# Kernel tuning notes

Hardware: AMD Instinct MI355X
Metric: run time of the kernel (lower is better)

## Reference

```python
import jax, jax.numpy as jnp
import numpy as np

B, N, D, H = 4, 2048, 256, 8
DK = D // H
SCALE = np.sqrt(DK).astype(np.float32)


def setup_inputs() -> dict:
    key = jax.random.key(0)
    ks = jax.random.split(key, 8)
    s = 1.0 / np.sqrt(D)
    return {
        "x": jax.random.normal(ks[0], (B, N, D), jnp.float32),
        "edge_weights": jax.random.normal(ks[1], (B, N, N), jnp.float32),
        "mask": jax.random.randint(ks[2], (B, N, N), 0, 2, jnp.int32),
        "w_q": jax.random.normal(ks[3], (D, D), jnp.float32) * s,
        "w_k": jax.random.normal(ks[4], (D, D), jnp.float32) * s,
        "w_v": jax.random.normal(ks[5], (D, D), jnp.float32) * s,
        "w_o": jax.random.normal(ks[6], (D, D), jnp.float32) * s,
        "b_o": jax.random.normal(ks[7], (D,), jnp.float32) * s,
    }


def reference(x, edge_weights, mask, w_q, w_k, w_v, w_o, b_o):
    # torch Linear: y = x @ W.T ; split into heads -> [B, H, N, DK]
    def split_heads(t):
        return t.reshape(B, N, H, DK).transpose(0, 2, 1, 3)

    Q = split_heads(x @ w_q.T)
    K = split_heads(x @ w_k.T)
    V = split_heads(x @ w_v.T)

    scores = jnp.einsum("bhnd,bhmd->bhnm", Q, K) / SCALE
    scores = scores + edge_weights[:, None, :, :]
    scores = jnp.where(mask[:, None, :, :] == 0, jnp.float32(-1e9), scores)
    attn = jax.nn.softmax(scores, axis=-1)  # dropout is identity in eval
    out = jnp.einsum("bhnm,bhmd->bhnd", attn, V)
    out = out.transpose(0, 2, 1, 3).reshape(B, N, D)
    return out @ w_o.T + b_o
```

## Files before the change

### kernel.cpp

```cpp
#include <hip/hip_runtime.h>

#define LOG2E 1.4426950408889634f
#define NEGBIG -3.0e38f

typedef float  f32x4  __attribute__((ext_vector_type(4)));
typedef float  f32x16 __attribute__((ext_vector_type(16)));
typedef short  bf16x8 __attribute__((ext_vector_type(8)));
typedef unsigned short u16x4 __attribute__((ext_vector_type(4)));
typedef int    i32x4  __attribute__((ext_vector_type(4)));
typedef unsigned int u32x2 __attribute__((ext_vector_type(2)));

__device__ __forceinline__ unsigned short f2bf(float f) {
  union { float f; unsigned u; } v; v.f = f;
  unsigned r = v.u + 0x7FFFu + ((v.u >> 16) & 1u);
  return (unsigned short)(r >> 16);
}

__device__ __forceinline__ unsigned cvtpk(float a, float b) {
  unsigned r;
  asm("v_cvt_pk_bf16_f32 %0, %1, %2" : "=v"(r) : "v"(a), "v"(b));
  return r;
}

__device__ __forceinline__ bf16x8 load_cvt8(const float* p) {
  f32x4 a = *(const f32x4*)p;
  f32x4 b = *(const f32x4*)(p + 4);
  bf16x8 r;
  r[0]=(short)f2bf(a[0]); r[1]=(short)f2bf(a[1]); r[2]=(short)f2bf(a[2]); r[3]=(short)f2bf(a[3]);
  r[4]=(short)f2bf(b[0]); r[5]=(short)f2bf(b[1]); r[6]=(short)f2bf(b[2]); r[7]=(short)f2bf(b[3]);
  return r;
}

__global__ __launch_bounds__(256) void qkv_kernel(
    const float* __restrict__ x,
    const float* __restrict__ wq, const float* __restrict__ wk, const float* __restrict__ wv,
    unsigned short* __restrict__ Qo, unsigned short* __restrict__ Ko,
    unsigned short* __restrict__ Vto)
{
  const int mode = blockIdx.y;
  const int n0   = blockIdx.x * 64;
  const int b    = n0 >> 11;
  const int nl0  = n0 & 2047;
  const int wave = threadIdx.x >> 6;
  const int lane = threadIdx.x & 63;
  const int li = lane & 15, qt = lane >> 4;

  f32x4 acc[4][4];
#pragma unroll
  for (int i = 0; i < 4; i++)
#pragma unroll
    for (int j = 0; j < 4; j++) acc[i][j] = (f32x4)0.0f;

  if (mode < 2) {
    const float* w = mode ? wk : wq;
    const float osc = mode ? 1.0f : (1.4426950408889634f / 5.656854249492381f);
#pragma unroll
    for (int ks = 0; ks < 8; ks++) {
      bf16x8 af[4], bfr[4];
#pragma unroll
      for (int dm = 0; dm < 4; dm++)
        af[dm] = load_cvt8(w + (size_t)(wave*64 + dm*16 + li)*256 + ks*32 + qt*8);
#pragma unroll
      for (int nf = 0; nf < 4; nf++)
        bfr[nf] = load_cvt8(x + (size_t)(n0 + nf*16 + li)*256 + ks*32 + qt*8);
#pragma unroll
      for (int dm = 0; dm < 4; dm++)
#pragma unroll
        for (int nf = 0; nf < 4; nf++)
          acc[dm][nf] = __builtin_amdgcn_mfma_f32_16x16x32_bf16(af[dm], bfr[nf], acc[dm][nf], 0, 0, 0);
    }
#pragma unroll
    for (int dm = 0; dm < 4; dm++) {
      const int dbase = wave*64 + dm*16 + qt*4;
      const int h = dbase >> 5, dk = dbase & 31;
#pragma unroll
      for (int nf = 0; nf < 4; nf++) {
        const int nl = nl0 + nf*16 + li;
        u16x4 o;
#pragma unroll
        for (int r = 0; r < 4; r++) o[r] = f2bf(acc[dm][nf][r] * osc);
        if (mode == 0) {
          *(u16x4*)(Qo + ((size_t)(b*8 + h)*2048 + nl)*32 + dk) = o;
        } else {
          const size_t addr = (size_t)(b*8 + h)*65536
              + (size_t)(nl >> 5)*1024 + (size_t)((dk >> 4) & 1)*512
              + (size_t)((nl & 31) + 32*((dk >> 3) & 1))*8 + (dk & 7);
          *(u16x4*)(Ko + addr) = o;
        }
      }
    }
  } else {
#pragma unroll
    for (int ks = 0; ks < 8; ks++) {
      bf16x8 af[4], bfr[4];
#pragma unroll
      for (int nm = 0; nm < 4; nm++)
        af[nm] = load_cvt8(x + (size_t)(n0 + nm*16 + li)*256 + ks*32 + qt*8);
#pragma unroll
      for (int df = 0; df < 4; df++)
        bfr[df] = load_cvt8(wv + (size_t)(wave*64 + df*16 + li)*256 + ks*32 + qt*8);
#pragma unroll
      for (int nm = 0; nm < 4; nm++)
#pragma unroll
        for (int df = 0; df < 4; df++)
          acc[nm][df] = __builtin_amdgcn_mfma_f32_16x16x32_bf16(af[nm], bfr[df], acc[nm][df], 0, 0, 0);
    }
#pragma unroll
    for (int nm = 0; nm < 4; nm++) {
      const int nl = nl0 + nm*16 + qt*4;
#pragma unroll
      for (int df = 0; df < 4; df++) {
        const int d = wave*64 + df*16 + li;
        const int h = d >> 5, dv = d & 31;
        u16x4 o;
#pragma unroll
        for (int r = 0; r < 4; r++) o[r] = f2bf(acc[nm][df][r]);
        const size_t addr = (size_t)(b*8 + h)*65536
            + (size_t)(nl >> 5)*1024 + (size_t)((nl >> 4) & 1)*512
            + (size_t)(((nl >> 3) & 1)*32 + dv)*8 + (nl & 7);
        *(u16x4*)(Vto + addr) = o;
      }
    }
  }
}

__global__ __launch_bounds__(512, 2) void attn_kernel(
    const unsigned short* __restrict__ Qg,
    const unsigned short* __restrict__ Kf,
    const unsigned short* __restrict__ Vf,
    const float* __restrict__ edge,
    const int*   __restrict__ mask,
    unsigned short* __restrict__ Og)
{
  __shared__ __attribute__((aligned(16))) float me_s[2][4096];

  const int bid = blockIdx.x;
  const int b  = (bid >> 1) & 3;
  const int qi = ((bid >> 3) << 1) | (bid & 1);
  const int q0 = qi * 32;
  const int tid  = threadIdx.x;
  const int wave = tid >> 6;
  const int lane = tid & 63;
  const int ql = lane & 31, hi = lane >> 5;
  const int h = wave;

  const unsigned short* qbase = Qg + ((size_t)(b*8 + h)*2048 + q0)*32;
  const unsigned short* kf = Kf + (size_t)(b*8 + h)*65536 + lane*8;
  const unsigned short* vf = Vf + (size_t)(b*8 + h)*65536 + lane*8;

  const int q_s = tid >> 4;
  const int k4  = (tid & 15) * 4;
  const float* eaddr = edge + ((size_t)b*2048 + q0 + q_s)*2048 + k4;
  const int*   maddr = mask + ((size_t)b*2048 + q0 + q_s)*2048 + k4;
  const int sC2  = (((k4 & 31) >> 3) * 2) + ((k4 >> 2) & 1);
  const int widx = (k4 >> 5)*1024 + (sC2*32 + (q_s ^ sC2))*4;
  int rix[4];
#pragma unroll
  for (int rg = 0; rg < 4; rg++) {
    const int C2 = rg*2 + hi;
    rix[rg] = (C2*32 + (ql ^ C2)) * 4;
  }

  const bf16x8 qf0 = *(const bf16x8*)(qbase + (size_t)ql*32 +  0 + hi*8);
  const bf16x8 qf1 = *(const bf16x8*)(qbase + (size_t)ql*32 + 16 + hi*8);

  {
    f32x4 e0 = *(const f32x4*)eaddr;
    i32x4 m0 = *(const i32x4*)maddr;
    f32x4 e1 = *(const f32x4*)(eaddr + 64);
    i32x4 m1 = *(const i32x4*)(maddr + 64);
    f32x4 v0, v1;
#pragma unroll
    for (int r = 0; r < 4; r++) v0[r] = m0[r] ? e0[r]*LOG2E : NEGBIG;
#pragma unroll
    for (int r = 0; r < 4; r++) v1[r] = m1[r] ? e1[r]*LOG2E : NEGBIG;
    *(f32x4*)&me_s[0][widx] = v0;
    *(f32x4*)&me_s[0][widx + 2048] = v1;
  }
  __syncthreads();

  f32x4 se0 = *(const f32x4*)(eaddr + 128);
  i32x4 sm0 = *(const i32x4*)(maddr + 128);
  f32x4 se1 = *(const f32x4*)(eaddr + 192);
  i32x4 sm1 = *(const i32x4*)(maddr + 192);

  bf16x8 kXa = *(const bf16x8*)(kf);
  bf16x8 kXb = *(const bf16x8*)(kf + 512);
  bf16x8 kYa, kYb;

  float lsum = 0.f;
  f32x16 oacc = (f32x16)0.0f;

  union CU { f32x16 v; f32x4 q[4]; };

#define PV_KS(SV, HALF, VA)                                                   \
  {                                                                           \
    unsigned a0 = cvtpk(SV[(HALF)*8+0], SV[(HALF)*8+1]);                      \
    unsigned a1 = cvtpk(SV[(HALF)*8+2], SV[(HALF)*8+3]);                      \
    unsigned b0 = cvtpk(SV[(HALF)*8+4], SV[(HALF)*8+5]);                      \
    unsigned b1 = cvtpk(SV[(HALF)*8+6], SV[(HALF)*8+7]);                      \
    u32x2 p0 = __builtin_amdgcn_permlane32_swap(a0, b0, false, false);        \
    u32x2 p1 = __builtin_amdgcn_permlane32_swap(a1, b1, false, false);        \
    i32x4 pw4;                                                                \
    pw4[0] = (int)p0[0]; pw4[1] = (int)p1[0];                                 \
    pw4[2] = (int)p0[1]; pw4[3] = (int)p1[1];                                 \
    const bf16x8 pf = __builtin_bit_cast(bf16x8, pw4);                        \
    oacc = __builtin_amdgcn_mfma_f32_32x32x16_bf16(VA, pf, oacc, 0, 0, 0);    \
  }

#define GROUP(KB, T, KCa, KCb, KNa, KNb)                                      \
  {                                                                           \
    const size_t nxt = (size_t)(((KB) + 1) & 63) * 1024;                      \
    KNa = *(const bf16x8*)(kf + nxt);                                         \
    KNb = *(const bf16x8*)(kf + nxt + 512);                                   \
    const bf16x8 vA0 = *(const bf16x8*)(vf + (size_t)(KB)*1024);              \
    const bf16x8 vA1 = *(const bf16x8*)(vf + (size_t)(KB)*1024 + 512);        \
    CU c;                                                                     \
    _Pragma("unroll")                                                         \
    for (int rg = 0; rg < 4; rg++)                                            \
      c.q[rg] = *(const f32x4*)(mb + (T)*1024 + rix[rg]);                     \
    f32x16 s = __builtin_amdgcn_mfma_f32_32x32x16_bf16(KCa, qf0, c.v, 0, 0, 0); \
    s = __builtin_amdgcn_mfma_f32_32x32x16_bf16(KCb, qf1, s, 0, 0, 0);        \
    _Pragma("unroll")                                                         \
    for (int i = 0; i < 16; i++) s[i] = __builtin_amdgcn_exp2f(s[i]);         \
    {                                                                         \
      float r0 = 0.f, r1 = 0.f, r2 = 0.f, r3 = 0.f;                           \
      _Pragma("unroll")                                                       \
      for (int i = 0; i < 4; i++) {                                           \
        r0 += s[4*i]; r1 += s[4*i+1]; r2 += s[4*i+2]; r3 += s[4*i+3];         \
      }                                                                       \
      lsum += (r0 + r1) + (r2 + r3);                                          \
    }                                                                         \
    PV_KS(s, 0, vA0)                                                          \
    PV_KS(s, 1, vA1)                                                          \
  }

  for (int p = 0; p < 16; ++p) {
    const float* mb = &me_s[p & 1][0];
    if (p < 15) {
      f32x4 v0, v1;
#pragma unroll
      for (int r = 0; r < 4; r++) v0[r] = sm0[r] ? se0[r]*LOG2E : NEGBIG;
#pragma unroll
      for (int r = 0; r < 4; r++) v1[r] = sm1[r] ? se1[r]*LOG2E : NEGBIG;
      *(f32x4*)&me_s[(p + 1) & 1][widx] = v0;
      *(f32x4*)&me_s[(p + 1) & 1][widx + 2048] = v1;
    }
    if (p < 14) {
      se0 = *(const f32x4*)(eaddr + (p + 2)*128);
      sm0 = *(const i32x4*)(maddr + (p + 2)*128);
      se1 = *(const f32x4*)(eaddr + (p + 2)*128 + 64);
      sm1 = *(const i32x4*)(maddr + (p + 2)*128 + 64);
    }
    const int g0 = p * 4;
    GROUP(g0,     0, kXa, kXb, kYa, kYb)
    GROUP(g0 + 1, 1, kYa, kYb, kXa, kXb)
    GROUP(g0 + 2, 2, kXa, kXb, kYa, kYb)
    GROUP(g0 + 3, 3, kYa, kYb, kXa, kXb)
    __syncthreads();
  }
#undef GROUP
#undef PV_KS

  const float ltot = lsum + __shfl_xor(lsum, 32);
  const float rl = 1.0f / ltot;
#pragma unroll
  for (int rg = 0; rg < 4; rg++) {
    u16x4 o;
#pragma unroll
    for (int r = 0; r < 4; r++) o[r] = f2bf(oacc[rg*4 + r] * rl);
    *(u16x4*)(Og + ((size_t)(b*2048 + q0 + ql))*256 + h*32 + rg*8 + hi*4) = o;
  }
}

__global__ __launch_bounds__(256) void proj_kernel(
    const unsigned short* __restrict__ O,
    const float* __restrict__ wo, const float* __restrict__ bo,
    float* __restrict__ Y)
{
  const int n0   = blockIdx.x * 64;
  const int wave = threadIdx.x >> 6;
  const int lane = threadIdx.x & 63;
  const int li = lane & 15, qt = lane >> 4;

  f32x4 acc[4][4];
#pragma unroll
  for (int i = 0; i < 4; i++)
#pragma unroll
    for (int j = 0; j < 4; j++) acc[i][j] = (f32x4)0.0f;

#pragma unroll
  for (int ks = 0; ks < 8; ks++) {
    bf16x8 af[4], bfr[4];
#pragma unroll
    for (int dm = 0; dm < 4; dm++)
      af[dm] = load_cvt8(wo + (size_t)(wave*64 + dm*16 + li)*256 + ks*32 + qt*8);
#pragma unroll
    for (int nf = 0; nf < 4; nf++)
      bfr[nf] = *(const bf16x8*)(O + (size_t)(n0 + nf*16 + li)*256 + ks*32 + qt*8);
#pragma unroll
    for (int dm = 0; dm < 4; dm++)
#pragma unroll
      for (int nf = 0; nf < 4; nf++)
        acc[dm][nf] = __builtin_amdgcn_mfma_f32_16x16x32_bf16(af[dm], bfr[nf], acc[dm][nf], 0, 0, 0);
  }

#pragma unroll
  for (int dm = 0; dm < 4; dm++) {
    const int d0 = wave*64 + dm*16 + qt*4;
    const f32x4 bo4 = *(const f32x4*)(bo + d0);
#pragma unroll
    for (int nf = 0; nf < 4; nf++) {
      const int n = n0 + nf*16 + li;
      f32x4 y = acc[dm][nf] + bo4;
      *(f32x4*)(Y + (size_t)n*256 + d0) = y;
    }
  }
}

extern "C" void kernel_launch(void* const* d_in, const int* in_sizes, int n_in,
                              void* d_out, int out_size, void* d_ws, size_t ws_size,
                              hipStream_t stream) {
  const float* x  = (const float*)d_in[0];
  const float* ew = (const float*)d_in[1];
  const int*   mk = (const int*)d_in[2];
  const float* wq = (const float*)d_in[3];
  const float* wk = (const float*)d_in[4];
  const float* wv = (const float*)d_in[5];
  const float* wo = (const float*)d_in[6];
  const float* bo = (const float*)d_in[7];
  float* y = (float*)d_out;

  unsigned short* Q  = (unsigned short*)d_ws;
  unsigned short* Kf = Q  + 2097152;
  unsigned short* Vf = Kf + 2097152;
  unsigned short* O  = Vf + 2097152;

  qkv_kernel<<<dim3(128, 3), 256, 0, stream>>>(x, wq, wk, wv, Q, Kf, Vf);
  attn_kernel<<<256, 512, 0, stream>>>(Q, Kf, Vf, ew, mk, O);
  proj_kernel<<<128, 256, 0, stream>>>(O, wo, bo, y);
}
```

Before: 94.97 us.

## Split attention block into two four-head halves with 256 threads each

The attention kernel now launches 512 blocks of 256 threads instead of 256 blocks of 512. Each block handles four heads for its 32-query tile, selected by the low block-id bit. Each thread stages twice as many edge/mask elements into shared memory so the 256 threads still fill the same tile. This gives finer-grained blocks and possibly better occupancy or scheduling. In exchange, every edge/mask tile is now read and converted by two blocks instead of one, doubling that global traffic and conversion work.

```diff
diff --git a/kernel.cpp b/kernel.cpp
--- a/kernel.cpp
+++ b/kernel.cpp
@@ -124,7 +124,7 @@
   }
 }
 
-__global__ __launch_bounds__(512, 2) void attn_kernel(
+__global__ __launch_bounds__(256, 2) void attn_kernel(
     const unsigned short* __restrict__ Qg,
     const unsigned short* __restrict__ Kf,
     const unsigned short* __restrict__ Vf,
@@ -136,13 +136,14 @@
 
   const int bid = blockIdx.x;
   const int b  = (bid >> 1) & 3;
-  const int qi = ((bid >> 3) << 1) | (bid & 1);
+  const int hg = bid & 1;
+  const int qi = bid >> 3;
   const int q0 = qi * 32;
   const int tid  = threadIdx.x;
   const int wave = tid >> 6;
   const int lane = tid & 63;
   const int ql = lane & 31, hi = lane >> 5;
-  const int h = wave;
+  const int h = hg*4 + wave;
 
   const unsigned short* qbase = Qg + ((size_t)(b*8 + h)*2048 + q0)*32;
   const unsigned short* kf = Kf + (size_t)(b*8 + h)*65536 + lane*8;
@@ -152,6 +153,8 @@
   const int k4  = (tid & 15) * 4;
   const float* eaddr = edge + ((size_t)b*2048 + q0 + q_s)*2048 + k4;
   const int*   maddr = mask + ((size_t)b*2048 + q0 + q_s)*2048 + k4;
+  const float* eaddr2 = eaddr + 16*2048;
+  const int*   maddr2 = maddr + 16*2048;
   const int sC2  = (((k4 & 31) >> 3) * 2) + ((k4 >> 2) & 1);
   const int widx = (k4 >> 5)*1024 + (sC2*32 + (q_s ^ sC2))*4;
   int rix[4];
@@ -164,25 +167,35 @@
   const bf16x8 qf0 = *(const bf16x8*)(qbase + (size_t)ql*32 +  0 + hi*8);
   const bf16x8 qf1 = *(const bf16x8*)(qbase + (size_t)ql*32 + 16 + hi*8);
 
+#define STAGE_CONV_WRITE(BUF, E00, M00, E10, M10, E01, M01, E11, M11)         \
+  {                                                                           \
+    f32x4 w00, w10, w01, w11;                                                 \
+    _Pragma("unroll")                                                         \
+    for (int r = 0; r < 4; r++) {                                             \
+      w00[r] = M00[r] ? E00[r]*LOG2E : NEGBIG;                                \
+      w10[r] = M10[r] ? E10[r]*LOG2E : NEGBIG;                                \
+      w01[r] = M01[r] ? E01[r]*LOG2E : NEGBIG;                                \
+      w11[r] = M11[r] ? E11[r]*LOG2E : NEGBIG;                                \
+    }                                                                         \
+    *(f32x4*)&me_s[BUF][widx]        = w00;                                   \
+    *(f32x4*)&me_s[BUF][widx + 64]   = w10;                                   \
+    *(f32x4*)&me_s[BUF][widx + 2048] = w01;                                   \
+    *(f32x4*)&me_s[BUF][widx + 2112] = w11;                                   \
+  }
+
   {
-    f32x4 e0 = *(const f32x4*)eaddr;
-    i32x4 m0 = *(const i32x4*)maddr;
-    f32x4 e1 = *(const f32x4*)(eaddr + 64);
-    i32x4 m1 = *(const i32x4*)(maddr + 64);
-    f32x4 v0, v1;
-#pragma unroll
-    for (int r = 0; r < 4; r++) v0[r] = m0[r] ? e0[r]*LOG2E : NEGBIG;
-#pragma unroll
-    for (int r = 0; r < 4; r++) v1[r] = m1[r] ? e1[r]*LOG2E : NEGBIG;
-    *(f32x4*)&me_s[0][widx] = v0;
-    *(f32x4*)&me_s[0][widx + 2048] = v1;
+    f32x4 e00 = *(const f32x4*)eaddr;        i32x4 m00 = *(const i32x4*)maddr;
+    f32x4 e10 = *(const f32x4*)eaddr2;       i32x4 m10 = *(const i32x4*)maddr2;
+    f32x4 e01 = *(const f32x4*)(eaddr + 64); i32x4 m01 = *(const i32x4*)(maddr + 64);
+    f32x4 e11 = *(const f32x4*)(eaddr2 + 64);i32x4 m11 = *(const i32x4*)(maddr2 + 64);
+    STAGE_CONV_WRITE(0, e00, m00, e10, m10, e01, m01, e11, m11)
   }
   __syncthreads();
 
-  f32x4 se0 = *(const f32x4*)(eaddr + 128);
-  i32x4 sm0 = *(const i32x4*)(maddr + 128);
-  f32x4 se1 = *(const f32x4*)(eaddr + 192);
-  i32x4 sm1 = *(const i32x4*)(maddr + 192);
+  f32x4 se00 = *(const f32x4*)(eaddr + 128);  i32x4 sm00 = *(const i32x4*)(maddr + 128);
+  f32x4 se10 = *(const f32x4*)(eaddr2 + 128); i32x4 sm10 = *(const i32x4*)(maddr2 + 128);
+  f32x4 se01 = *(const f32x4*)(eaddr + 192);  i32x4 sm01 = *(const i32x4*)(maddr + 192);
+  f32x4 se11 = *(const f32x4*)(eaddr2 + 192); i32x4 sm11 = *(const i32x4*)(maddr2 + 192);
 
   bf16x8 kXa = *(const bf16x8*)(kf);
   bf16x8 kXb = *(const bf16x8*)(kf + 512);
@@ -238,19 +251,14 @@
   for (int p = 0; p < 16; ++p) {
     const float* mb = &me_s[p & 1][0];
     if (p < 15) {
-      f32x4 v0, v1;
-#pragma unroll
-      for (int r = 0; r < 4; r++) v0[r] = sm0[r] ? se0[r]*LOG2E : NEGBIG;
-#pragma unroll
-      for (int r = 0; r < 4; r++) v1[r] = sm1[r] ? se1[r]*LOG2E : NEGBIG;
-      *(f32x4*)&me_s[(p + 1) & 1][widx] = v0;
-      *(f32x4*)&me_s[(p + 1) & 1][widx + 2048] = v1;
+      STAGE_CONV_WRITE((p + 1) & 1, se00, sm00, se10, sm10, se01, sm01, se11, sm11)
     }
     if (p < 14) {
-      se0 = *(const f32x4*)(eaddr + (p + 2)*128);
-      sm0 = *(const i32x4*)(maddr + (p + 2)*128);
-      se1 = *(const f32x4*)(eaddr + (p + 2)*128 + 64);
-      sm1 = *(const i32x4*)(maddr + (p + 2)*128 + 64);
+      const int ofs = (p + 2)*128;
+      se00 = *(const f32x4*)(eaddr + ofs);       sm00 = *(const i32x4*)(maddr + ofs);
+      se10 = *(const f32x4*)(eaddr2 + ofs);      sm10 = *(const i32x4*)(maddr2 + ofs);
+      se01 = *(const f32x4*)(eaddr + ofs + 64);  sm01 = *(const i32x4*)(maddr + ofs + 64);
+      se11 = *(const f32x4*)(eaddr2 + ofs + 64); sm11 = *(const i32x4*)(maddr2 + ofs + 64);
     }
     const int g0 = p * 4;
     GROUP(g0,     0, kXa, kXb, kYa, kYb)
@@ -261,6 +269,7 @@
   }
 #undef GROUP
 #undef PV_KS
+#undef STAGE_CONV_WRITE
 
   const float ltot = lsum + __shfl_xor(lsum, 32);
   const float rl = 1.0f / ltot;
@@ -337,6 +346,6 @@
   unsigned short* O  = Vf + 2097152;
 
   qkv_kernel<<<dim3(128, 3), 256, 0, stream>>>(x, wq, wk, wv, Q, Kf, Vf);
-  attn_kernel<<<256, 512, 0, stream>>>(Q, Kf, Vf, ew, mk, O);
+  attn_kernel<<<512, 256, 0, stream>>>(Q, Kf, Vf, ew, mk, O);
   proj_kernel<<<128, 256, 0, stream>>>(O, wo, bo, y);
 }
```

Result: slower. 103.8 us (+9.3%).

## Split attention key range across two wave groups per block and merge partials

Applied to the files above, without the earlier changes.

Doubles the attention block to 1024 threads: each head is served by two waves, each handling half of the key range, with separate staged edge/mask tiles in shared memory. At the end, the second-half waves write their partial output accumulators and row sums to LDS, and the first-half waves add them before normalising and storing. The aim is to halve the serial loop length per wave and raise latency hiding within a block. The cost is double the shared memory, one extra merge barrier, and launch bounds that allow only one block per CU, which may cap register use.

```diff
diff --git a/kernel.cpp b/kernel.cpp
--- a/kernel.cpp
+++ b/kernel.cpp
@@ -124,7 +124,7 @@
   }
 }
 
-__global__ __launch_bounds__(512, 2) void attn_kernel(
+__global__ __launch_bounds__(1024, 1) void attn_kernel(
     const unsigned short* __restrict__ Qg,
     const unsigned short* __restrict__ Kf,
     const unsigned short* __restrict__ Vf,
@@ -132,7 +132,7 @@
     const int*   __restrict__ mask,
     unsigned short* __restrict__ Og)
 {
-  __shared__ __attribute__((aligned(16))) float me_s[2][4096];
+  __shared__ __attribute__((aligned(16))) float me_s[2][2][4096];
 
   const int bid = blockIdx.x;
   const int b  = (bid >> 1) & 3;
@@ -142,16 +142,19 @@
   const int wave = tid >> 6;
   const int lane = tid & 63;
   const int ql = lane & 31, hi = lane >> 5;
-  const int h = wave;
+  const int h  = wave & 7;
+  const int kh = wave >> 3;
 
   const unsigned short* qbase = Qg + ((size_t)(b*8 + h)*2048 + q0)*32;
-  const unsigned short* kf = Kf + (size_t)(b*8 + h)*65536 + lane*8;
-  const unsigned short* vf = Vf + (size_t)(b*8 + h)*65536 + lane*8;
-
-  const int q_s = tid >> 4;
-  const int k4  = (tid & 15) * 4;
-  const float* eaddr = edge + ((size_t)b*2048 + q0 + q_s)*2048 + k4;
-  const int*   maddr = mask + ((size_t)b*2048 + q0 + q_s)*2048 + k4;
+  const unsigned short* kf = Kf + (size_t)(b*8 + h)*65536 + (size_t)kh*32768 + lane*8;
+  const unsigned short* vf = Vf + (size_t)(b*8 + h)*65536 + (size_t)kh*32768 + lane*8;
+
+  const int th  = tid >> 9;
+  const int t9  = tid & 511;
+  const int q_s = t9 >> 4;
+  const int k4  = (t9 & 15) * 4;
+  const float* eaddr = edge + ((size_t)b*2048 + q0 + q_s)*2048 + th*1024 + k4;
+  const int*   maddr = mask + ((size_t)b*2048 + q0 + q_s)*2048 + th*1024 + k4;
   const int sC2  = (((k4 & 31) >> 3) * 2) + ((k4 >> 2) & 1);
   const int widx = (k4 >> 5)*1024 + (sC2*32 + (q_s ^ sC2))*4;
   int rix[4];
@@ -174,8 +177,8 @@
     for (int r = 0; r < 4; r++) v0[r] = m0[r] ? e0[r]*LOG2E : NEGBIG;
 #pragma unroll
     for (int r = 0; r < 4; r++) v1[r] = m1[r] ? e1[r]*LOG2E : NEGBIG;
-    *(f32x4*)&me_s[0][widx] = v0;
-    *(f32x4*)&me_s[0][widx + 2048] = v1;
+    *(f32x4*)&me_s[0][th][widx] = v0;
+    *(f32x4*)&me_s[0][th][widx + 2048] = v1;
   }
   __syncthreads();
 
@@ -210,7 +213,7 @@
 
 #define GROUP(KB, T, KCa, KCb, KNa, KNb)                                      \
   {                                                                           \
-    const size_t nxt = (size_t)(((KB) + 1) & 63) * 1024;                      \
+    const size_t nxt = (size_t)(((KB) + 1) & 31) * 1024;                      \
     KNa = *(const bf16x8*)(kf + nxt);                                         \
     KNb = *(const bf16x8*)(kf + nxt + 512);                                   \
     const bf16x8 vA0 = *(const bf16x8*)(vf + (size_t)(KB)*1024);              \
@@ -235,22 +238,23 @@
     PV_KS(s, 1, vA1)                                                          \
   }
 
-  for (int p = 0; p < 16; ++p) {
-    const float* mb = &me_s[p & 1][0];
-    if (p < 15) {
+  for (int p = 0; p < 8; ++p) {
+    const float* mb = &me_s[p & 1][kh][0];
+    if (p < 7) {
       f32x4 v0, v1;
 #pragma unroll
       for (int r = 0; r < 4; r++) v0[r] = sm0[r] ? se0[r]*LOG2E : NEGBIG;
 #pragma unroll
       for (int r = 0; r < 4; r++) v1[r] = sm1[r] ? se1[r]*LOG2E : NEGBIG;
-      *(f32x4*)&me_s[(p + 1) & 1][widx] = v0;
-      *(f32x4*)&me_s[(p + 1) & 1][widx + 2048] = v1;
-    }
-    if (p < 14) {
-      se0 = *(const f32x4*)(eaddr + (p + 2)*128);
-      sm0 = *(const i32x4*)(maddr + (p + 2)*128);
-      se1 = *(const f32x4*)(eaddr + (p + 2)*128 + 64);
-      sm1 = *(const i32x4*)(maddr + (p + 2)*128 + 64);
+      *(f32x4*)&me_s[(p + 1) & 1][th][widx] = v0;
+      *(f32x4*)&me_s[(p + 1) & 1][th][widx + 2048] = v1;
+    }
+    if (p < 6) {
+      const int ofs = (p + 2)*128;
+      se0 = *(const f32x4*)(eaddr + ofs);
+      sm0 = *(const i32x4*)(maddr + ofs);
+      se1 = *(const f32x4*)(eaddr + ofs + 64);
+      sm1 = *(const i32x4*)(maddr + ofs + 64);
     }
     const int g0 = p * 4;
     GROUP(g0,     0, kXa, kXb, kYa, kYb)
@@ -262,14 +266,27 @@
 #undef GROUP
 #undef PV_KS
 
-  const float ltot = lsum + __shfl_xor(lsum, 32);
-  const float rl = 1.0f / ltot;
-#pragma unroll
-  for (int rg = 0; rg < 4; rg++) {
-    u16x4 o;
-#pragma unroll
-    for (int r = 0; r < 4; r++) o[r] = f2bf(oacc[rg*4 + r] * rl);
-    *(u16x4*)(Og + ((size_t)(b*2048 + q0 + ql))*256 + h*32 + rg*8 + hi*4) = o;
+  float* mrg = &me_s[0][0][0];
+  const int mbase = h*1088 + lane*17;
+  if (kh == 1) {
+#pragma unroll
+    for (int i = 0; i < 16; i++) mrg[mbase + i] = oacc[i];
+    mrg[mbase + 16] = lsum;
+  }
+  __syncthreads();
+  if (kh == 0) {
+#pragma unroll
+    for (int i = 0; i < 16; i++) oacc[i] += mrg[mbase + i];
+    lsum += mrg[mbase + 16];
+    const float ltot = lsum + __shfl_xor(lsum, 32);
+    const float rl = 1.0f / ltot;
+#pragma unroll
+    for (int rg = 0; rg < 4; rg++) {
+      u16x4 o;
+#pragma unroll
+      for (int r = 0; r < 4; r++) o[r] = f2bf(oacc[rg*4 + r] * rl);
+      *(u16x4*)(Og + ((size_t)(b*2048 + q0 + ql))*256 + h*32 + rg*8 + hi*4) = o;
+    }
   }
 }
 
@@ -337,6 +354,6 @@
   unsigned short* O  = Vf + 2097152;
 
   qkv_kernel<<<dim3(128, 3), 256, 0, stream>>>(x, wq, wk, wv, Q, Kf, Vf);
-  attn_kernel<<<256, 512, 0, stream>>>(Q, Kf, Vf, ew, mk, O);
+  attn_kernel<<<256, 1024, 0, stream>>>(Q, Kf, Vf, ew, mk, O);
   proj_kernel<<<128, 256, 0, stream>>>(O, wo, bo, y);
 }
```

Result: slower. 105.5 us (+11.1%).

## Fuse output projection into attention kernel epilogue via LDS-staged O tile

Applied to the files above, without the earlier changes.

Removes the separate proj_kernel launch and the global round-trip of the bf16 attention output. Each attention block writes its normalized 32x256 output tile to shared memory, synchronizes, and then its 8 waves compute a 32-column slice of the W_o projection plus bias directly to Y. This saves one kernel launch and the O write/read. In exchange, every block reloads and converts the fp32 W_o slice, and the extra LDS may reduce occupancy.

```diff
diff --git a/kernel.cpp b/kernel.cpp
--- a/kernel.cpp
+++ b/kernel.cpp
@@ -130,9 +130,12 @@
     const unsigned short* __restrict__ Vf,
     const float* __restrict__ edge,
     const int*   __restrict__ mask,
-    unsigned short* __restrict__ Og)
+    const float* __restrict__ wo,
+    const float* __restrict__ bo,
+    float* __restrict__ Y)
 {
   __shared__ __attribute__((aligned(16))) float me_s[2][4096];
+  __shared__ __attribute__((aligned(16))) unsigned short o_lds[32][264];
 
   const int bid = blockIdx.x;
   const int b  = (bid >> 1) & 3;
@@ -262,58 +265,51 @@
 #undef GROUP
 #undef PV_KS
 
-  const float ltot = lsum + __shfl_xor(lsum, 32);
-  const float rl = 1.0f / ltot;
-#pragma unroll
-  for (int rg = 0; rg < 4; rg++) {
-    u16x4 o;
-#pragma unroll
-    for (int r = 0; r < 4; r++) o[r] = f2bf(oacc[rg*4 + r] * rl);
-    *(u16x4*)(Og + ((size_t)(b*2048 + q0 + ql))*256 + h*32 + rg*8 + hi*4) = o;
-  }
-}
-
-__global__ __launch_bounds__(256) void proj_kernel(
-    const unsigned short* __restrict__ O,
-    const float* __restrict__ wo, const float* __restrict__ bo,
-    float* __restrict__ Y)
-{
-  const int n0   = blockIdx.x * 64;
-  const int wave = threadIdx.x >> 6;
-  const int lane = threadIdx.x & 63;
-  const int li = lane & 15, qt = lane >> 4;
-
-  f32x4 acc[4][4];
-#pragma unroll
-  for (int i = 0; i < 4; i++)
-#pragma unroll
-    for (int j = 0; j < 4; j++) acc[i][j] = (f32x4)0.0f;
-
-#pragma unroll
-  for (int ks = 0; ks < 8; ks++) {
-    bf16x8 af[4], bfr[4];
-#pragma unroll
-    for (int dm = 0; dm < 4; dm++)
-      af[dm] = load_cvt8(wo + (size_t)(wave*64 + dm*16 + li)*256 + ks*32 + qt*8);
-#pragma unroll
-    for (int nf = 0; nf < 4; nf++)
-      bfr[nf] = *(const bf16x8*)(O + (size_t)(n0 + nf*16 + li)*256 + ks*32 + qt*8);
-#pragma unroll
-    for (int dm = 0; dm < 4; dm++)
-#pragma unroll
-      for (int nf = 0; nf < 4; nf++)
-        acc[dm][nf] = __builtin_amdgcn_mfma_f32_16x16x32_bf16(af[dm], bfr[nf], acc[dm][nf], 0, 0, 0);
-  }
-
-#pragma unroll
-  for (int dm = 0; dm < 4; dm++) {
-    const int d0 = wave*64 + dm*16 + qt*4;
-    const f32x4 bo4 = *(const f32x4*)(bo + d0);
-#pragma unroll
-    for (int nf = 0; nf < 4; nf++) {
-      const int n = n0 + nf*16 + li;
-      f32x4 y = acc[dm][nf] + bo4;
-      *(f32x4*)(Y + (size_t)n*256 + d0) = y;
+  {
+    const float ltot = lsum + __shfl_xor(lsum, 32);
+    const float rl = 1.0f / ltot;
+#pragma unroll
+    for (int rg = 0; rg < 4; rg++) {
+      u16x4 o;
+#pragma unroll
+      for (int r = 0; r < 4; r++) o[r] = f2bf(oacc[rg*4 + r] * rl);
+      *(u16x4*)&o_lds[ql][h*32 + rg*8 + hi*4] = o;
+    }
+  }
+  __syncthreads();
+
+  {
+    const int li = lane & 15, qt = lane >> 4;
+    f32x4 acc2[2][2];
+#pragma unroll
+    for (int i = 0; i < 2; i++)
+#pragma unroll
+      for (int j = 0; j < 2; j++) acc2[i][j] = (f32x4)0.0f;
+#pragma unroll
+    for (int ks = 0; ks < 8; ks++) {
+      bf16x8 af[2], bfr[2];
+#pragma unroll
+      for (int df = 0; df < 2; df++)
+        af[df] = load_cvt8(wo + (size_t)(wave*32 + df*16 + li)*256 + ks*32 + qt*8);
+#pragma unroll
+      for (int nf = 0; nf < 2; nf++)
+        bfr[nf] = *(const bf16x8*)&o_lds[nf*16 + li][ks*32 + qt*8];
+#pragma unroll
+      for (int df = 0; df < 2; df++)
+#pragma unroll
+        for (int nf = 0; nf < 2; nf++)
+          acc2[df][nf] = __builtin_amdgcn_mfma_f32_16x16x32_bf16(af[df], bfr[nf], acc2[df][nf], 0, 0, 0);
+    }
+#pragma unroll
+    for (int df = 0; df < 2; df++) {
+      const int d0 = wave*32 + df*16 + qt*4;
+      const f32x4 bo4 = *(const f32x4*)(bo + d0);
+#pragma unroll
+      for (int nf = 0; nf < 2; nf++) {
+        const int n = nf*16 + li;
+        f32x4 y = acc2[df][nf] + bo4;
+        *(f32x4*)(Y + ((size_t)(b*2048 + q0 + n))*256 + d0) = y;
+      }
     }
   }
 }
@@ -334,9 +330,7 @@
   unsigned short* Q  = (unsigned short*)d_ws;
   unsigned short* Kf = Q  + 2097152;
   unsigned short* Vf = Kf + 2097152;
-  unsigned short* O  = Vf + 2097152;
 
   qkv_kernel<<<dim3(128, 3), 256, 0, stream>>>(x, wq, wk, wv, Q, Kf, Vf);
-  attn_kernel<<<256, 512, 0, stream>>>(Q, Kf, Vf, ew, mk, O);
-  proj_kernel<<<128, 256, 0, stream>>>(O, wo, bo, y);
-}
+  attn_kernel<<<256, 512, 0, stream>>>(Q, Kf, Vf, ew, mk, wo, bo, y);
+}
```

New measurement: 84.38 us. 1.13x faster.
